# Kernel optimization log

Measured on AMD Instinct MI355X. Metric: run time of the kernel, lower is better.

The kernel has to match this reference:

```python
import jax, jax.numpy as jnp
import numpy as np

QMIN, QMAX = -128, 127  # int8 range, n_bit = 8


def setup_inputs() -> dict:
    key = jax.random.key(0)
    k1, k2, k3, k4 = jax.random.split(key, 4)
    B, S, IN, OUT = 4, 2048, 4096, 4096
    x = jax.random.normal(k1, (B, S, IN), dtype=jnp.float32)
    weight = jax.random.randint(k2, (OUT, IN), QMIN, QMAX + 1, dtype=jnp.int32).astype(jnp.int8)
    scales = (jax.random.uniform(k3, (OUT,), dtype=jnp.float32) * 0.02 + 1e-3)
    zeros = jax.random.randint(k4, (OUT,), -10, 11, dtype=jnp.int32).astype(jnp.float32)
    return {"x": x, "weight": weight, "scales": scales, "zeros": zeros}


def _per_token_dynamic_quant(x):
    # torchao per_token_dynamic_quant: asymmetric int8 quantize per token
    # (over last dim), then dequantize back to float.
    mn = jnp.minimum(jnp.min(x, axis=-1, keepdims=True), 0.0)
    mx = jnp.maximum(jnp.max(x, axis=-1, keepdims=True), 0.0)
    eps = jnp.finfo(jnp.float32).eps
    scale = jnp.maximum((mx - mn) / (QMAX - QMIN), eps)
    zp = jnp.clip(QMIN - jnp.round(mn / scale), QMIN, QMAX)
    q = jnp.clip(jnp.round(x / scale) + zp, QMIN, QMAX)
    return (q - zp) * scale


def reference(x, weight, scales, zeros):
    x_dq = _per_token_dynamic_quant(x.astype(jnp.float32))
    # per-channel (axis 0 = out_features) weight dequant:
    # w_dq[o, i] = (w_int8[o, i] - zeros[o]) * scales[o]
    w_dq = (weight.astype(jnp.float32) - zeros[:, None]) * scales[:, None]
    # F.linear: x @ w_dq.T -> [B, S, OUT]
    return jnp.einsum('bsi,oi->bso', x_dq, w_dq)
```

## Files before the change

### kernel.cpp

```cpp
#include <hip/hip_runtime.h>
#include <stdint.h>

typedef int   v4i __attribute__((ext_vector_type(4)));
typedef float v4f __attribute__((ext_vector_type(4)));

#define TOK_M 8192
#define DIM_K 4096
#define DIM_N 4096

#define GL(src, dst)                                                                   \
  __builtin_amdgcn_global_load_lds((const __attribute__((address_space(1))) void*)(src), \
                                   (__attribute__((address_space(3))) void*)(dst), 16, 0, 0)

__global__ __launch_bounds__(256) void k_pack_w(const int* __restrict__ w,
                                                int8_t* __restrict__ wq,
                                                float* __restrict__ wsumf) {
    __shared__ int sred[4];
    const int row = blockIdx.x;
    const int tid = threadIdx.x;
    const int4* src = (const int4*)(w + (size_t)row * DIM_K);
    unsigned* dst = (unsigned*)(wq + (size_t)row * DIM_K);
    int sum = 0;
#pragma unroll
    for (int c = 0; c < 4; ++c) {
        int4 iv = src[c * 256 + tid];
        sum += iv.x + iv.y + iv.z + iv.w;
        unsigned p = (unsigned)(iv.x & 255) | ((unsigned)(iv.y & 255) << 8) |
                     ((unsigned)(iv.z & 255) << 16) | ((unsigned)(iv.w & 255) << 24);
        dst[c * 256 + tid] = p;
    }
#pragma unroll
    for (int off = 32; off; off >>= 1) sum += __shfl_xor(sum, off);
    if ((tid & 63) == 0) sred[tid >> 6] = sum;
    __syncthreads();
    if (tid == 0) wsumf[row] = (float)(sred[0] + sred[1] + sred[2] + sred[3]);
}

__global__ __launch_bounds__(256) void k_quant(const float* __restrict__ x,
                                               int8_t* __restrict__ q,
                                               float* __restrict__ sA,
                                               float* __restrict__ sB,
                                               float* __restrict__ sC) {
    __shared__ float redf[8];
    __shared__ int   redi[4];
    __shared__ float bcast[2];
    const int tok = blockIdx.x;
    const int tid = threadIdx.x;
    const v4f* xr = (const v4f*)(x + (size_t)tok * DIM_K);
    v4f v[4];
    float mn = 0.0f, mx = 0.0f;
#pragma unroll
    for (int c = 0; c < 4; ++c) {
        v[c] = xr[c * 256 + tid];
#pragma unroll
        for (int j = 0; j < 4; ++j) {
            mn = fminf(mn, v[c][j]);
            mx = fmaxf(mx, v[c][j]);
        }
    }
#pragma unroll
    for (int off = 32; off; off >>= 1) {
        mn = fminf(mn, __shfl_xor(mn, off));
        mx = fmaxf(mx, __shfl_xor(mx, off));
    }
    const int wid = tid >> 6;
    if ((tid & 63) == 0) { redf[wid] = mn; redf[4 + wid] = mx; }
    __syncthreads();
    if (tid == 0) {
        float m0 = fminf(fminf(redf[0], redf[1]), fminf(redf[2], redf[3]));
        float m1 = fmaxf(fmaxf(redf[4], redf[5]), fmaxf(redf[6], redf[7]));
        float scale = fmaxf((m1 - m0) / 255.0f, 1.1920928955078125e-07f);
        float zpf = -128.0f - rintf(m0 / scale);
        zpf = fminf(fmaxf(zpf, -128.0f), 127.0f);
        bcast[0] = scale; bcast[1] = zpf;
    }
    __syncthreads();
    const float scale = bcast[0];
    const float zpf   = bcast[1];
    const float inv   = 1.0f / scale;
    int qs = 0;
    unsigned* qo = (unsigned*)(q + (size_t)tok * DIM_K);
#pragma unroll
    for (int c = 0; c < 4; ++c) {
        unsigned p = 0;
#pragma unroll
        for (int j = 0; j < 4; ++j) {
            float qf = rintf(v[c][j] * inv) + zpf;
            qf = fminf(fmaxf(qf, -128.0f), 127.0f);
            int qi = (int)qf;
            qs += qi;
            p |= ((unsigned)(qi & 255)) << (8 * j);
        }
        qo[c * 256 + tid] = p;
    }
#pragma unroll
    for (int off = 32; off; off >>= 1) qs += __shfl_xor(qs, off);
    if ((tid & 63) == 0) redi[wid] = qs;
    __syncthreads();
    if (tid == 0) {
        int qtot = redi[0] + redi[1] + redi[2] + redi[3];
        sA[tok] = scale;
        sB[tok] = scale * zpf;
        sC[tok] = scale * ((float)qtot - 4096.0f * zpf);
    }
}

#define MFMA8(mI, afR)                                                                     \
    acc[mI][0] = __builtin_amdgcn_mfma_i32_16x16x64_i8(afR, bf0, acc[mI][0], 0, 0, 0);     \
    acc[mI][1] = __builtin_amdgcn_mfma_i32_16x16x64_i8(afR, bf1, acc[mI][1], 0, 0, 0);     \
    acc[mI][2] = __builtin_amdgcn_mfma_i32_16x16x64_i8(afR, bf2, acc[mI][2], 0, 0, 0);     \
    acc[mI][3] = __builtin_amdgcn_mfma_i32_16x16x64_i8(afR, bf3, acc[mI][3], 0, 0, 0);

__global__ __launch_bounds__(512, 2) void k_gemm(const int8_t* __restrict__ A,
                                                 const int8_t* __restrict__ B,
                                                 const float* __restrict__ sA,
                                                 const float* __restrict__ sB,
                                                 const float* __restrict__ sC,
                                                 const float* __restrict__ wsumf,
                                                 const float* __restrict__ scales,
                                                 const float* __restrict__ zeros,
                                                 float* __restrict__ out) {
    extern __shared__ int8_t lds[];
    const int tid = threadIdx.x;
    const int l = tid & 63;
    const int wid = tid >> 6;

    const int bswz = (blockIdx.x & 7) * 64 + (blockIdx.x >> 3);
    const int tm = (bswz & 31) * 256;
    const int tn = (bswz >> 5) * 256;

    const int sr  = tid >> 2;
    const int scg = (tid & 3) ^ ((tid >> 3) & 3);
    const int8_t* aS0 = A + (size_t)(tm + sr) * DIM_K + scg * 16;
    const int8_t* aS1 = A + (size_t)(tm + 128 + sr) * DIM_K + scg * 16;
    const int8_t* bS0 = B + (size_t)(tn + sr) * DIM_K + scg * 16;
    const int8_t* bS1 = B + (size_t)(tn + 128 + sr) * DIM_K + scg * 16;
    const int dA0 = tid * 16;
    const int dA1 = 8192 + tid * 16;

    const int i  = l & 15;
    const int ch = l >> 4;
    const int pos = ch ^ ((i >> 1) & 3);
    const int wm = (wid >> 2) * 128;
    const int wn = (wid & 3) * 64;
    const int aOff = (wm + i) * 64 + pos * 16;
    const int bOff = 16384 + (wn + i) * 64 + pos * 16;

    v4i acc[8][4] = {};

    GL(aS0, lds + dA0);          GL(aS1, lds + dA1);
    GL(bS0, lds + 16384 + dA0);  GL(bS1, lds + 16384 + dA1);
    GL(aS0 + 64, lds + 32768 + dA0);          GL(aS1 + 64, lds + 32768 + dA1);
    GL(bS0 + 64, lds + 32768 + 16384 + dA0);  GL(bS1 + 64, lds + 32768 + 16384 + dA1);
    asm volatile("s_waitcnt vmcnt(4)" ::: "memory");
    __builtin_amdgcn_s_barrier();

    int cb = 0, sb = 2;
    for (int kt = 0; kt < 64; ++kt) {
        const int koff = kt * 64 + 128;
        int8_t* Sc = lds + cb * 32768;
        int8_t* St = lds + sb * 32768;
        const bool doStage = (kt < 62);
        v4i bf0, bf1, bf2, bf3;

        if (doStage) GL(aS0 + koff, St + dA0);
        bf0 = *(const v4i*)(Sc + bOff);
        bf1 = *(const v4i*)(Sc + bOff + 1024);
        bf2 = *(const v4i*)(Sc + bOff + 2048);
        bf3 = *(const v4i*)(Sc + bOff + 3072);
        {
            v4i a0 = *(const v4i*)(Sc + aOff);
            v4i a1 = *(const v4i*)(Sc + aOff + 1024);
            __builtin_amdgcn_sched_barrier(0);
            __builtin_amdgcn_s_setprio(1);
            MFMA8(0, a0) MFMA8(1, a1)
            __builtin_amdgcn_s_setprio(0);
            __builtin_amdgcn_sched_barrier(0);
        }
        __builtin_amdgcn_s_barrier();

        if (doStage) GL(aS1 + koff, St + dA1);
        {
            v4i a2 = *(const v4i*)(Sc + aOff + 2048);
            v4i a3 = *(const v4i*)(Sc + aOff + 3072);
            __builtin_amdgcn_sched_barrier(0);
            __builtin_amdgcn_s_setprio(1);
            MFMA8(2, a2) MFMA8(3, a3)
            __builtin_amdgcn_s_setprio(0);
            __builtin_amdgcn_sched_barrier(0);
        }
        __builtin_amdgcn_s_barrier();

        if (doStage) GL(bS0 + koff, St + 16384 + dA0);
        {
            v4i a4 = *(const v4i*)(Sc + aOff + 4096);
            v4i a5 = *(const v4i*)(Sc + aOff + 5120);
            __builtin_amdgcn_sched_barrier(0);
            __builtin_amdgcn_s_setprio(1);
            MFMA8(4, a4) MFMA8(5, a5)
            __builtin_amdgcn_s_setprio(0);
            __builtin_amdgcn_sched_barrier(0);
        }
        __builtin_amdgcn_s_barrier();

        if (doStage) GL(bS1 + koff, St + 16384 + dA1);
        {
            v4i a6 = *(const v4i*)(Sc + aOff + 6144);
            v4i a7 = *(const v4i*)(Sc + aOff + 7168);
            __builtin_amdgcn_sched_barrier(0);
            __builtin_amdgcn_s_setprio(1);
            MFMA8(6, a6) MFMA8(7, a7)
            __builtin_amdgcn_s_setprio(0);
            __builtin_amdgcn_sched_barrier(0);
        }
        if (kt < 62) { asm volatile("s_waitcnt vmcnt(4)" ::: "memory"); }
        else         { asm volatile("s_waitcnt vmcnt(0)" ::: "memory"); }
        __builtin_amdgcn_s_barrier();

        cb = (cb == 2) ? 0 : cb + 1;
        sb = (sb == 2) ? 0 : sb + 1;
    }

    const int gr0 = tm + wm + ch * 4;
    const int gc0 = tn + wn + i;
    float scl[4], zr[4], wsm[4];
#pragma unroll
    for (int n = 0; n < 4; ++n) {
        const int gc = gc0 + n * 16;
        scl[n] = scales[gc]; zr[n] = zeros[gc]; wsm[n] = wsumf[gc];
    }
#pragma unroll
    for (int m = 0; m < 8; ++m) {
#pragma unroll
        for (int j = 0; j < 4; ++j) {
            const int gr = gr0 + m * 16 + j;
            const float ra = sA[gr], rb = sB[gr], rc = sC[gr];
            float* orow = out + (size_t)gr * DIM_N;
#pragma unroll
            for (int n = 0; n < 4; ++n)
                orow[gc0 + n * 16] =
                    scl[n] * (ra * (float)acc[m][n][j] - rb * wsm[n] - rc * zr[n]);
        }
    }
}

extern "C" void kernel_launch(void* const* d_in, const int* in_sizes, int n_in,
                              void* d_out, int out_size, void* d_ws, size_t ws_size,
                              hipStream_t stream) {
    const float* x      = (const float*)d_in[0];
    const int*   w      = (const int*)d_in[1];
    const float* scales = (const float*)d_in[2];
    const float* zeros  = (const float*)d_in[3];
    float* out = (float*)d_out;

    uint8_t* ws = (uint8_t*)d_ws;
    int8_t* q  = (int8_t*)ws;
    int8_t* wq = (int8_t*)(ws + (size_t)TOK_M * DIM_K);
    float* fbuf = (float*)(ws + (size_t)TOK_M * DIM_K + (size_t)DIM_N * DIM_K);
    float* sA    = fbuf;
    float* sB    = fbuf + TOK_M;
    float* sC    = fbuf + 2 * TOK_M;
    float* wsumf = fbuf + 3 * TOK_M;

    k_pack_w<<<DIM_N, 256, 0, stream>>>(w, wq, wsumf);
    k_quant<<<TOK_M, 256, 0, stream>>>(x, q, sA, sB, sC);
    k_gemm<<<512, 512, 98304, stream>>>(q, wq, sA, sB, sC, wsumf, scales, zeros, out);
}
```

Measured before the change: 416.8 us.

## Restructure int8 GEMM main loop into two phases and remap block-to-XCD tiles

The K-loop goes from four sub-phases, each issuing one global-to-LDS load and 8 MFMAs, to two phases, each issuing two loads and 16 MFMAs, with the barriers placed before the MFMA bursts. Block indices are remapped so each XCD handles an 8x8 patch of output tiles, which should improve L2 reuse of A and B rows within an XCD. Fewer barriers per iteration should cut sync overhead, at the cost of holding four A fragments live at once and producing a burstier load issue pattern.

```diff
diff --git a/kernel.cpp b/kernel.cpp
--- a/kernel.cpp
+++ b/kernel.cpp
@@ -105,11 +105,11 @@
     }
 }
 
-#define MFMA8(mI, afR)                                                                     \
-    acc[mI][0] = __builtin_amdgcn_mfma_i32_16x16x64_i8(afR, bf0, acc[mI][0], 0, 0, 0);     \
-    acc[mI][1] = __builtin_amdgcn_mfma_i32_16x16x64_i8(afR, bf1, acc[mI][1], 0, 0, 0);     \
-    acc[mI][2] = __builtin_amdgcn_mfma_i32_16x16x64_i8(afR, bf2, acc[mI][2], 0, 0, 0);     \
-    acc[mI][3] = __builtin_amdgcn_mfma_i32_16x16x64_i8(afR, bf3, acc[mI][3], 0, 0, 0);
+#define MM4(AF, M)                                                                  \
+    acc[M][0] = __builtin_amdgcn_mfma_i32_16x16x64_i8(AF, bf0, acc[M][0], 0, 0, 0); \
+    acc[M][1] = __builtin_amdgcn_mfma_i32_16x16x64_i8(AF, bf1, acc[M][1], 0, 0, 0); \
+    acc[M][2] = __builtin_amdgcn_mfma_i32_16x16x64_i8(AF, bf2, acc[M][2], 0, 0, 0); \
+    acc[M][3] = __builtin_amdgcn_mfma_i32_16x16x64_i8(AF, bf3, acc[M][3], 0, 0, 0);
 
 __global__ __launch_bounds__(512, 2) void k_gemm(const int8_t* __restrict__ A,
                                                  const int8_t* __restrict__ B,
@@ -125,9 +125,10 @@
     const int l = tid & 63;
     const int wid = tid >> 6;
 
-    const int bswz = (blockIdx.x & 7) * 64 + (blockIdx.x >> 3);
-    const int tm = (bswz & 31) * 256;
-    const int tn = (bswz >> 5) * 256;
+    const int xcd = blockIdx.x & 7;
+    const int idx = blockIdx.x >> 3;
+    const int tm = ((xcd >> 1) * 8 + (idx & 7)) * 256;
+    const int tn = ((xcd & 1) * 8 + (idx >> 3)) * 256;
 
     const int sr  = tid >> 2;
     const int scg = (tid & 3) ^ ((tid >> 3) & 3);
@@ -161,58 +162,36 @@
         int8_t* Sc = lds + cb * 32768;
         int8_t* St = lds + sb * 32768;
         const bool doStage = (kt < 62);
-        v4i bf0, bf1, bf2, bf3;
-
-        if (doStage) GL(aS0 + koff, St + dA0);
+        v4i af0, af1, af2, af3, bf0, bf1, bf2, bf3;
+
+        if (doStage) { GL(aS0 + koff, St + dA0); GL(aS1 + koff, St + dA1); }
         bf0 = *(const v4i*)(Sc + bOff);
         bf1 = *(const v4i*)(Sc + bOff + 1024);
         bf2 = *(const v4i*)(Sc + bOff + 2048);
         bf3 = *(const v4i*)(Sc + bOff + 3072);
-        {
-            v4i a0 = *(const v4i*)(Sc + aOff);
-            v4i a1 = *(const v4i*)(Sc + aOff + 1024);
-            __builtin_amdgcn_sched_barrier(0);
-            __builtin_amdgcn_s_setprio(1);
-            MFMA8(0, a0) MFMA8(1, a1)
-            __builtin_amdgcn_s_setprio(0);
-            __builtin_amdgcn_sched_barrier(0);
-        }
-        __builtin_amdgcn_s_barrier();
-
-        if (doStage) GL(aS1 + koff, St + dA1);
-        {
-            v4i a2 = *(const v4i*)(Sc + aOff + 2048);
-            v4i a3 = *(const v4i*)(Sc + aOff + 3072);
-            __builtin_amdgcn_sched_barrier(0);
-            __builtin_amdgcn_s_setprio(1);
-            MFMA8(2, a2) MFMA8(3, a3)
-            __builtin_amdgcn_s_setprio(0);
-            __builtin_amdgcn_sched_barrier(0);
-        }
-        __builtin_amdgcn_s_barrier();
-
-        if (doStage) GL(bS0 + koff, St + 16384 + dA0);
-        {
-            v4i a4 = *(const v4i*)(Sc + aOff + 4096);
-            v4i a5 = *(const v4i*)(Sc + aOff + 5120);
-            __builtin_amdgcn_sched_barrier(0);
-            __builtin_amdgcn_s_setprio(1);
-            MFMA8(4, a4) MFMA8(5, a5)
-            __builtin_amdgcn_s_setprio(0);
-            __builtin_amdgcn_sched_barrier(0);
-        }
-        __builtin_amdgcn_s_barrier();
-
-        if (doStage) GL(bS1 + koff, St + 16384 + dA1);
-        {
-            v4i a6 = *(const v4i*)(Sc + aOff + 6144);
-            v4i a7 = *(const v4i*)(Sc + aOff + 7168);
-            __builtin_amdgcn_sched_barrier(0);
-            __builtin_amdgcn_s_setprio(1);
-            MFMA8(6, a6) MFMA8(7, a7)
-            __builtin_amdgcn_s_setprio(0);
-            __builtin_amdgcn_sched_barrier(0);
-        }
+        af0 = *(const v4i*)(Sc + aOff);
+        af1 = *(const v4i*)(Sc + aOff + 1024);
+        af2 = *(const v4i*)(Sc + aOff + 2048);
+        af3 = *(const v4i*)(Sc + aOff + 3072);
+        __builtin_amdgcn_sched_barrier(0);
+        __builtin_amdgcn_s_barrier();
+        __builtin_amdgcn_s_setprio(1);
+        MM4(af0, 0) MM4(af1, 1) MM4(af2, 2) MM4(af3, 3)
+        __builtin_amdgcn_s_setprio(0);
+        __builtin_amdgcn_sched_barrier(0);
+        __builtin_amdgcn_s_barrier();
+
+        if (doStage) { GL(bS0 + koff, St + 16384 + dA0); GL(bS1 + koff, St + 16384 + dA1); }
+        af0 = *(const v4i*)(Sc + aOff + 4096);
+        af1 = *(const v4i*)(Sc + aOff + 5120);
+        af2 = *(const v4i*)(Sc + aOff + 6144);
+        af3 = *(const v4i*)(Sc + aOff + 7168);
+        __builtin_amdgcn_sched_barrier(0);
+        __builtin_amdgcn_s_barrier();
+        __builtin_amdgcn_s_setprio(1);
+        MM4(af0, 4) MM4(af1, 5) MM4(af2, 6) MM4(af3, 7)
+        __builtin_amdgcn_s_setprio(0);
+        __builtin_amdgcn_sched_barrier(0);
         if (kt < 62) { asm volatile("s_waitcnt vmcnt(4)" ::: "memory"); }
         else         { asm volatile("s_waitcnt vmcnt(0)" ::: "memory"); }
         __builtin_amdgcn_s_barrier();
```

After: 407.4 us. 2.3% less time.
